# Optimization experiments

Measured on AMD Instinct MI355X. Metric: run time of the kernel, lower is better.

The kernel has to match this reference:

```python
import jax, jax.numpy as jnp
import numpy as np

N = 128   # system size (number of sequential RNN steps)
B = 8192  # batch of samples
H = 128   # hidden units per layer (units=[128,128])
D = 2     # input_dim (spin up/down one-hot)


def setup_inputs() -> dict:
    key = jax.random.key(0)
    ks = jax.random.split(key, 11)
    s = 1.0 / np.sqrt(H)  # torch nn.RNNCell/Linear default U(-1/sqrt(H), 1/sqrt(H))
    bits = jax.random.randint(ks[0], (N, B), 0, D)
    samples = jax.nn.one_hot(bits, D, dtype=jnp.float32)  # (N, B, D) one-hot spins
    u = lambda k, shp: jax.random.uniform(k, shp, jnp.float32, -s, s)
    return {
        "samples": samples,
        "W_ih0": u(ks[1], (H, D)), "b_ih0": u(ks[2], (H,)),
        "W_hh0": u(ks[3], (H, H)), "b_hh0": u(ks[4], (H,)),
        "W_ih1": u(ks[5], (H, H)), "b_ih1": u(ks[6], (H,)),
        "W_hh1": u(ks[7], (H, H)), "b_hh1": u(ks[8], (H,)),
        "W_dense": u(ks[9], (D, H)), "b_dense": u(ks[10], (D,)),
    }


def reference(samples, W_ih0, b_ih0, W_hh0, b_hh0,
              W_ih1, b_ih1, W_hh1, b_hh1, W_dense, b_dense):
    # Faithful jax port of RNN_wavefunction.log_prob:
    # p_t = <softmax(dense(h1_t)), s_t>; returns sum_t log p_t with shape (1, B).
    # For one-hot s_t, log(sum(prob*s_t)) == sum(s_t * log_softmax(logits)) (stable form).
    Bsz = samples.shape[1]
    # input at step t is the sampled spin from step t-1; zeros at t=0
    inputs = jnp.concatenate(
        [jnp.zeros((1, Bsz, D), samples.dtype), samples[:-1]], axis=0)
    h0 = jnp.zeros((Bsz, H), samples.dtype)
    h1 = jnp.zeros((Bsz, H), samples.dtype)

    def step(carry, xs):
        h0, h1 = carry
        x_t, s_t = xs  # x_t: (B, D) prev spin one-hot, s_t: (B, D) current spin
        # nn.RNNCell: h' = tanh(x W_ih^T + b_ih + h W_hh^T + b_hh)
        h0 = jnp.tanh(x_t @ W_ih0.T + b_ih0 + h0 @ W_hh0.T + b_hh0)
        h1 = jnp.tanh(h0 @ W_ih1.T + b_ih1 + h1 @ W_hh1.T + b_hh1)
        logits = h1 @ W_dense.T + b_dense           # (B, 2)
        logp = jax.nn.log_softmax(logits, axis=-1)
        lp_t = jnp.sum(logp * s_t, axis=-1)          # (B,) = log p(s_t)
        return (h0, h1), lp_t

    _, lps = jax.lax.scan(step, (h0, h1), (inputs, samples))  # lps: (N, B)
    return jnp.sum(lps, axis=0, keepdims=True)  # (1, B), matches torch keepdim=True
```

## Files before the change

### kernel.cpp

```cpp
#include <hip/hip_runtime.h>
#include <hip/hip_bf16.h>


#define NSTEP 128
#define BTOT  8192
#define HID   128
#define MB    16
#define NBLK  (BTOT / MB)
#define NTHR  256

typedef __attribute__((ext_vector_type(8))) short bf16x8;
typedef __attribute__((ext_vector_type(4))) float f32x4;
typedef __attribute__((ext_vector_type(2))) float f32x2;
typedef __attribute__((ext_vector_type(2))) unsigned uint32x2;

__device__ __forceinline__ short f2bf(float v) {
    unsigned u = __builtin_bit_cast(unsigned, v);
    u += 0x7FFFu + ((u >> 16) & 1u);
    return (short)(u >> 16);
}
__device__ __forceinline__ unsigned pk2bf(float a, float b) {
    unsigned ua = __builtin_bit_cast(unsigned, a);
    unsigned ub = __builtin_bit_cast(unsigned, b);
    ua += 0x7FFFu + ((ua >> 16) & 1u);
    ub += 0x7FFFu + ((ub >> 16) & 1u);
    return (ua >> 16) | (ub & 0xFFFF0000u);
}
__device__ __forceinline__ f32x2 tanh2(f32x2 x) {
    f32x2 z = x * 2.885390081777927f;
    f32x2 e;
    e.x = __builtin_exp2f(z.x);
    e.y = __builtin_exp2f(z.y);
    f32x2 d = e + 1.0f;
    f32x2 r;
    r.x = __builtin_amdgcn_rcpf(d.x);
    r.y = __builtin_amdgcn_rcpf(d.y);
    return r * -2.0f + 1.0f;
}

__global__ __launch_bounds__(NTHR, 2) void rnn_wf_kernel(
    const float* __restrict__ samples,
    const float* __restrict__ Wih0,
    const float* __restrict__ bih0,
    const float* __restrict__ Whh0,
    const float* __restrict__ bhh0,
    const float* __restrict__ Wih1,
    const float* __restrict__ bih1,
    const float* __restrict__ Whh1,
    const float* __restrict__ bhh1,
    const float* __restrict__ Wd,
    const float* __restrict__ bd,
    float* __restrict__ out)
{
    __shared__ short sH0[2][MB * HID];
    __shared__ short sH1[2][MB * HID];
    __shared__ unsigned sMask[NSTEP];

    const int tid  = threadIdx.x;
    const int b0   = blockIdx.x * MB;
    const int w    = tid >> 6;
    const int lane = tid & 63;
    const int q    = lane >> 4;
    const int c    = lane & 15;
    const int nb   = w * 32;

    if (tid < NSTEP) {
        unsigned msk = 0;
        #pragma unroll
        for (int m = 0; m < MB; ++m) {
            float e1 = samples[((size_t)tid * BTOT + b0 + m) * 2 + 1];
            if (e1 > 0.5f) msk |= (1u << m);
        }
        sMask[tid] = msk;
    }

    bf16x8 fhh0[2][4], fih1[2][4], fhh1[2][4];
    #pragma unroll
    for (int nt = 0; nt < 2; ++nt) {
        const int nn = nb + nt * 16 + c;
        #pragma unroll
        for (int kb = 0; kb < 4; ++kb) {
            const int off = nn * HID + kb * 32 + q * 8;
            bf16x8 v0, v1, v2;
            #pragma unroll
            for (int j = 0; j < 8; ++j) {
                v0[j] = f2bf(Whh0[off + j]);
                v1[j] = f2bf(Wih1[off + j]);
                v2[j] = f2bf(Whh1[off + j]);
            }
            fhh0[nt][kb] = v0; fih1[nt][kb] = v1; fhh1[nt][kb] = v2;
        }
    }
    bf16x8 fwd[4];
    #pragma unroll
    for (int kb = 0; kb < 4; ++kb) {
        bf16x8 v;
        #pragma unroll
        for (int j = 0; j < 8; ++j)
            v[j] = (c < 2) ? f2bf(Wd[c * HID + kb * 32 + q * 8 + j]) : (short)0;
        fwd[kb] = v;
    }
    f32x4 pA0, pA1, pB0, pB1, b0v0, b0v1, b1v0, b1v1;
    #pragma unroll
    for (int r = 0; r < 4; ++r) {
        const int n0 = nb + q * 4 + r;
        const int n1 = n0 + 16;
        const float bb0 = bih0[n0] + bhh0[n0];
        const float bb1 = bih0[n1] + bhh0[n1];
        b0v0[r] = bb0;                    b0v1[r] = bb1;
        pA0[r] = bb0 + Wih0[n0 * 2 + 0];  pA1[r] = bb1 + Wih0[n1 * 2 + 0];
        pB0[r] = bb0 + Wih0[n0 * 2 + 1];  pB1[r] = bb1 + Wih0[n1 * 2 + 1];
        b1v0[r] = bih1[n0] + bhh1[n0];    b1v1[r] = bih1[n1] + bhh1[n1];
    }
    const f32x4 bdv = {bd[0], bd[1], 0.f, 0.f};

    int ra[4];
    #pragma unroll
    for (int kb = 0; kb < 4; ++kb)
        ra[kb] = c * HID + (((kb * 4 + q) ^ c) << 3);
    int wa0 = c * HID + (((4 * w + (q >> 1)) ^ c) << 3) + ((q & 1) << 2);
    int wa1 = c * HID + (((4 * w + 2 + (q >> 1)) ^ c) << 3) + ((q & 1) << 2);

    float lp = 0.0f;
    bool bmPrev = false;

    auto storeH = [&](short* buf, const f32x4& a0, const f32x4& a1) {
        f32x2 t00 = tanh2((f32x2){a0[0], a0[1]});
        f32x2 t01 = tanh2((f32x2){a0[2], a0[3]});
        f32x2 t10 = tanh2((f32x2){a1[0], a1[1]});
        f32x2 t11 = tanh2((f32x2){a1[2], a1[3]});
        uint32x2 v0 = {pk2bf(t00.x, t00.y), pk2bf(t01.x, t01.y)};
        uint32x2 v1 = {pk2bf(t10.x, t10.y), pk2bf(t11.x, t11.y)};
        *reinterpret_cast<uint32x2*>(&buf[wa0]) = v0;
        *reinterpret_cast<uint32x2*>(&buf[wa1]) = v1;
    };
    auto lpAdd = [&](const f32x4& aL, bool bit) {
        const float l0 = aL[0], l1 = aL[1];
        const float lc = bit ? l1 : l0;
        const float lo = bit ? l0 : l1;
        const float ed = __builtin_exp2f((lo - lc) * 1.4426950408889634f);
        lp -= 0.6931471805599453f * __builtin_log2f(1.0f + ed);
    };

    __syncthreads();
    storeH(sH0[1], b0v0, b0v1);
    __syncthreads();

    {
        const bool bmIn = (sMask[0] >> c) & 1u;
        bf16x8 f0[4];
        #pragma unroll
        for (int kb = 0; kb < 4; ++kb)
            f0[kb] = *reinterpret_cast<const bf16x8*>(&sH0[1][ra[kb]]);
        f32x4 a00 = bmIn ? pB0 : pA0;
        f32x4 a01 = bmIn ? pB1 : pA1;
        f32x4 a10 = b1v0, a11 = b1v1;
        #pragma unroll
        for (int kb = 0; kb < 4; ++kb) {
            a00 = __builtin_amdgcn_mfma_f32_16x16x32_bf16(fhh0[0][kb], f0[kb], a00, 0, 0, 0);
            a01 = __builtin_amdgcn_mfma_f32_16x16x32_bf16(fhh0[1][kb], f0[kb], a01, 0, 0, 0);
            a10 = __builtin_amdgcn_mfma_f32_16x16x32_bf16(fih1[0][kb], f0[kb], a10, 0, 0, 0);
            a11 = __builtin_amdgcn_mfma_f32_16x16x32_bf16(fih1[1][kb], f0[kb], a11, 0, 0, 0);
        }
        storeH(sH0[0], a00, a01);
        storeH(sH1[0], a10, a11);
        bmPrev = bmIn;
        __syncthreads();
    }

    auto stepMain = [&](int i, const short* r0, const short* r1,
                        short* w0b, short* w1b) {
        const bool bmIn = (sMask[i - 1] >> c) & 1u;
        bf16x8 f0[4], f1[4];
        #pragma unroll
        for (int kb = 0; kb < 4; ++kb) {
            f0[kb] = *reinterpret_cast<const bf16x8*>(&r0[ra[kb]]);
            f1[kb] = *reinterpret_cast<const bf16x8*>(&r1[ra[kb]]);
        }
        f32x4 a00 = bmIn ? pB0 : pA0;
        f32x4 a01 = bmIn ? pB1 : pA1;
        f32x4 a10 = b1v0, a11 = b1v1;
        f32x4 aL  = bdv;
        #pragma unroll
        for (int kb = 0; kb < 4; ++kb) {
            a00 = __builtin_amdgcn_mfma_f32_16x16x32_bf16(fhh0[0][kb], f0[kb], a00, 0, 0, 0);
            a01 = __builtin_amdgcn_mfma_f32_16x16x32_bf16(fhh0[1][kb], f0[kb], a01, 0, 0, 0);
            a10 = __builtin_amdgcn_mfma_f32_16x16x32_bf16(fhh1[0][kb], f1[kb], a10, 0, 0, 0);
            a11 = __builtin_amdgcn_mfma_f32_16x16x32_bf16(fhh1[1][kb], f1[kb], a11, 0, 0, 0);
            aL  = __builtin_amdgcn_mfma_f32_16x16x32_bf16(fwd[kb],     f1[kb], aL,  0, 0, 0);
        }
        #pragma unroll
        for (int kb = 0; kb < 4; ++kb) {
            a10 = __builtin_amdgcn_mfma_f32_16x16x32_bf16(fih1[0][kb], f0[kb], a10, 0, 0, 0);
            a11 = __builtin_amdgcn_mfma_f32_16x16x32_bf16(fih1[1][kb], f0[kb], a11, 0, 0, 0);
        }
        lpAdd(aL, bmPrev);
        bmPrev = bmIn;
        storeH(w0b, a00, a01);
        storeH(w1b, a10, a11);
        __syncthreads();
    };

    for (int i = 2; i < NSTEP; i += 2) {
        stepMain(i,     sH0[0], sH1[0], sH0[1], sH1[1]);
        stepMain(i + 1, sH0[1], sH1[1], sH0[0], sH1[0]);
    }

    {
        bf16x8 f0[4], f1[4];
        #pragma unroll
        for (int kb = 0; kb < 4; ++kb) {
            f0[kb] = *reinterpret_cast<const bf16x8*>(&sH0[0][ra[kb]]);
            f1[kb] = *reinterpret_cast<const bf16x8*>(&sH1[0][ra[kb]]);
        }
        f32x4 a10 = b1v0, a11 = b1v1;
        f32x4 aL  = bdv;
        #pragma unroll
        for (int kb = 0; kb < 4; ++kb) {
            a10 = __builtin_amdgcn_mfma_f32_16x16x32_bf16(fhh1[0][kb], f1[kb], a10, 0, 0, 0);
            a11 = __builtin_amdgcn_mfma_f32_16x16x32_bf16(fhh1[1][kb], f1[kb], a11, 0, 0, 0);
            aL  = __builtin_amdgcn_mfma_f32_16x16x32_bf16(fwd[kb],     f1[kb], aL,  0, 0, 0);
        }
        #pragma unroll
        for (int kb = 0; kb < 4; ++kb) {
            a10 = __builtin_amdgcn_mfma_f32_16x16x32_bf16(fih1[0][kb], f0[kb], a10, 0, 0, 0);
            a11 = __builtin_amdgcn_mfma_f32_16x16x32_bf16(fih1[1][kb], f0[kb], a11, 0, 0, 0);
        }
        lpAdd(aL, bmPrev);
        storeH(sH1[1], a10, a11);
        __syncthreads();
    }
    {
        f32x4 aL = bdv;
        #pragma unroll
        for (int kb = 0; kb < 4; ++kb) {
            bf16x8 f1 = *reinterpret_cast<const bf16x8*>(&sH1[1][ra[kb]]);
            aL = __builtin_amdgcn_mfma_f32_16x16x32_bf16(fwd[kb], f1, aL, 0, 0, 0);
        }
        lpAdd(aL, (sMask[NSTEP - 1] >> c) & 1u);
    }

    if (tid < 16)
        out[b0 + tid] = lp;
}

extern "C" void kernel_launch(void* const* d_in, const int* in_sizes, int n_in,
                              void* d_out, int out_size, void* d_ws, size_t ws_size,
                              hipStream_t stream) {
    rnn_wf_kernel<<<NBLK, NTHR, 0, stream>>>(
        (const float*)d_in[0],
        (const float*)d_in[1],
        (const float*)d_in[2],
        (const float*)d_in[3],
        (const float*)d_in[4],
        (const float*)d_in[5],
        (const float*)d_in[6],
        (const float*)d_in[7],
        (const float*)d_in[8],
        (const float*)d_in[9],
        (const float*)d_in[10],
        (float*)d_out);
}
```

Measured before the change: 263.2 us.

## Restrict dense logits to one wave and defer log-softmax to a parallel epilogue

Only wave 0 now computes the dense-layer MFMA each step, and it stores the logit difference to a shared buffer instead of doing exp/log on the serial critical path. A final epilogue spreads the 128 softplus evaluations per sample across all threads and reduces them with shuffles. The change also fuses the bias init into the first MFMA, swaps manual bf16 packing for the HIP packed conversion intrinsic, and shares one reciprocal across two tanh values. It adds about 8.7KB of LDS, which may affect occupancy, and introduces wave divergence inside each step.

```diff
diff --git a/kernel.cpp b/kernel.cpp
--- a/kernel.cpp
+++ b/kernel.cpp
@@ -19,23 +19,19 @@
     u += 0x7FFFu + ((u >> 16) & 1u);
     return (short)(u >> 16);
 }
-__device__ __forceinline__ unsigned pk2bf(float a, float b) {
-    unsigned ua = __builtin_bit_cast(unsigned, a);
-    unsigned ub = __builtin_bit_cast(unsigned, b);
-    ua += 0x7FFFu + ((ua >> 16) & 1u);
-    ub += 0x7FFFu + ((ub >> 16) & 1u);
-    return (ua >> 16) | (ub & 0xFFFF0000u);
+__device__ __forceinline__ unsigned cvt2bf(float a, float b) {
+    __hip_bfloat162 h2 = __float22bfloat162_rn(make_float2(a, b));
+    unsigned u; __builtin_memcpy(&u, &h2, sizeof(u));
+    return u;
 }
 __device__ __forceinline__ f32x2 tanh2(f32x2 x) {
     f32x2 z = x * 2.885390081777927f;
-    f32x2 e;
-    e.x = __builtin_exp2f(z.x);
-    e.y = __builtin_exp2f(z.y);
-    f32x2 d = e + 1.0f;
-    f32x2 r;
-    r.x = __builtin_amdgcn_rcpf(d.x);
-    r.y = __builtin_amdgcn_rcpf(d.y);
-    return r * -2.0f + 1.0f;
+    float e0 = __builtin_exp2f(z.x);
+    float e1 = __builtin_exp2f(z.y);
+    f32x2 d = {e0 + 1.0f, e1 + 1.0f};
+    float r = __builtin_amdgcn_rcpf(d.x * d.y);
+    f32x2 inv = {r * d.y, r * d.x};
+    return inv * -2.0f + 1.0f;
 }
 
 __global__ __launch_bounds__(NTHR, 2) void rnn_wf_kernel(
@@ -55,6 +51,7 @@
     __shared__ short sH0[2][MB * HID];
     __shared__ short sH1[2][MB * HID];
     __shared__ unsigned sMask[NSTEP];
+    __shared__ float sLd[NSTEP * 17];
 
     const int tid  = threadIdx.x;
     const int b0   = blockIdx.x * MB;
@@ -118,10 +115,9 @@
     #pragma unroll
     for (int kb = 0; kb < 4; ++kb)
         ra[kb] = c * HID + (((kb * 4 + q) ^ c) << 3);
-    int wa0 = c * HID + (((4 * w + (q >> 1)) ^ c) << 3) + ((q & 1) << 2);
-    int wa1 = c * HID + (((4 * w + 2 + (q >> 1)) ^ c) << 3) + ((q & 1) << 2);
-
-    float lp = 0.0f;
+    const int wa0 = c * HID + (((4 * w + (q >> 1)) ^ c) << 3) + ((q & 1) << 2);
+    const int wa1 = c * HID + (((4 * w + 2 + (q >> 1)) ^ c) << 3) + ((q & 1) << 2);
+
     bool bmPrev = false;
 
     auto storeH = [&](short* buf, const f32x4& a0, const f32x4& a1) {
@@ -129,18 +125,11 @@
         f32x2 t01 = tanh2((f32x2){a0[2], a0[3]});
         f32x2 t10 = tanh2((f32x2){a1[0], a1[1]});
         f32x2 t11 = tanh2((f32x2){a1[2], a1[3]});
-        uint32x2 v0 = {pk2bf(t00.x, t00.y), pk2bf(t01.x, t01.y)};
-        uint32x2 v1 = {pk2bf(t10.x, t10.y), pk2bf(t11.x, t11.y)};
+        uint32x2 v0 = {cvt2bf(t00.x, t00.y), cvt2bf(t01.x, t01.y)};
+        uint32x2 v1 = {cvt2bf(t10.x, t10.y), cvt2bf(t11.x, t11.y)};
         *reinterpret_cast<uint32x2*>(&buf[wa0]) = v0;
         *reinterpret_cast<uint32x2*>(&buf[wa1]) = v1;
     };
-    auto lpAdd = [&](const f32x4& aL, bool bit) {
-        const float l0 = aL[0], l1 = aL[1];
-        const float lc = bit ? l1 : l0;
-        const float lo = bit ? l0 : l1;
-        const float ed = __builtin_exp2f((lo - lc) * 1.4426950408889634f);
-        lp -= 0.6931471805599453f * __builtin_log2f(1.0f + ed);
-    };
 
     __syncthreads();
     storeH(sH0[1], b0v0, b0v1);
@@ -152,11 +141,12 @@
         #pragma unroll
         for (int kb = 0; kb < 4; ++kb)
             f0[kb] = *reinterpret_cast<const bf16x8*>(&sH0[1][ra[kb]]);
-        f32x4 a00 = bmIn ? pB0 : pA0;
-        f32x4 a01 = bmIn ? pB1 : pA1;
-        f32x4 a10 = b1v0, a11 = b1v1;
-        #pragma unroll
-        for (int kb = 0; kb < 4; ++kb) {
+        f32x4 a00 = __builtin_amdgcn_mfma_f32_16x16x32_bf16(fhh0[0][0], f0[0], bmIn ? pB0 : pA0, 0, 0, 0);
+        f32x4 a01 = __builtin_amdgcn_mfma_f32_16x16x32_bf16(fhh0[1][0], f0[0], bmIn ? pB1 : pA1, 0, 0, 0);
+        f32x4 a10 = __builtin_amdgcn_mfma_f32_16x16x32_bf16(fih1[0][0], f0[0], b1v0, 0, 0, 0);
+        f32x4 a11 = __builtin_amdgcn_mfma_f32_16x16x32_bf16(fih1[1][0], f0[0], b1v1, 0, 0, 0);
+        #pragma unroll
+        for (int kb = 1; kb < 4; ++kb) {
             a00 = __builtin_amdgcn_mfma_f32_16x16x32_bf16(fhh0[0][kb], f0[kb], a00, 0, 0, 0);
             a01 = __builtin_amdgcn_mfma_f32_16x16x32_bf16(fhh0[1][kb], f0[kb], a01, 0, 0, 0);
             a10 = __builtin_amdgcn_mfma_f32_16x16x32_bf16(fih1[0][kb], f0[kb], a10, 0, 0, 0);
@@ -177,24 +167,30 @@
             f0[kb] = *reinterpret_cast<const bf16x8*>(&r0[ra[kb]]);
             f1[kb] = *reinterpret_cast<const bf16x8*>(&r1[ra[kb]]);
         }
-        f32x4 a00 = bmIn ? pB0 : pA0;
-        f32x4 a01 = bmIn ? pB1 : pA1;
-        f32x4 a10 = b1v0, a11 = b1v1;
-        f32x4 aL  = bdv;
-        #pragma unroll
-        for (int kb = 0; kb < 4; ++kb) {
+        f32x4 a00 = __builtin_amdgcn_mfma_f32_16x16x32_bf16(fhh0[0][0], f0[0], bmIn ? pB0 : pA0, 0, 0, 0);
+        f32x4 a01 = __builtin_amdgcn_mfma_f32_16x16x32_bf16(fhh0[1][0], f0[0], bmIn ? pB1 : pA1, 0, 0, 0);
+        f32x4 a10 = __builtin_amdgcn_mfma_f32_16x16x32_bf16(fhh1[0][0], f1[0], b1v0, 0, 0, 0);
+        f32x4 a11 = __builtin_amdgcn_mfma_f32_16x16x32_bf16(fhh1[1][0], f1[0], b1v1, 0, 0, 0);
+        #pragma unroll
+        for (int kb = 1; kb < 4; ++kb) {
             a00 = __builtin_amdgcn_mfma_f32_16x16x32_bf16(fhh0[0][kb], f0[kb], a00, 0, 0, 0);
             a01 = __builtin_amdgcn_mfma_f32_16x16x32_bf16(fhh0[1][kb], f0[kb], a01, 0, 0, 0);
             a10 = __builtin_amdgcn_mfma_f32_16x16x32_bf16(fhh1[0][kb], f1[kb], a10, 0, 0, 0);
             a11 = __builtin_amdgcn_mfma_f32_16x16x32_bf16(fhh1[1][kb], f1[kb], a11, 0, 0, 0);
-            aL  = __builtin_amdgcn_mfma_f32_16x16x32_bf16(fwd[kb],     f1[kb], aL,  0, 0, 0);
         }
         #pragma unroll
         for (int kb = 0; kb < 4; ++kb) {
             a10 = __builtin_amdgcn_mfma_f32_16x16x32_bf16(fih1[0][kb], f0[kb], a10, 0, 0, 0);
             a11 = __builtin_amdgcn_mfma_f32_16x16x32_bf16(fih1[1][kb], f0[kb], a11, 0, 0, 0);
         }
-        lpAdd(aL, bmPrev);
+        if (w == 0) {
+            f32x4 aL = __builtin_amdgcn_mfma_f32_16x16x32_bf16(fwd[0], f1[0], bdv, 0, 0, 0);
+            #pragma unroll
+            for (int kb = 1; kb < 4; ++kb)
+                aL = __builtin_amdgcn_mfma_f32_16x16x32_bf16(fwd[kb], f1[kb], aL, 0, 0, 0);
+            if (q == 0)
+                sLd[(i - 2) * 17 + c] = bmPrev ? (aL[0] - aL[1]) : (aL[1] - aL[0]);
+        }
         bmPrev = bmIn;
         storeH(w0b, a00, a01);
         storeH(w1b, a10, a11);
@@ -213,35 +209,63 @@
             f0[kb] = *reinterpret_cast<const bf16x8*>(&sH0[0][ra[kb]]);
             f1[kb] = *reinterpret_cast<const bf16x8*>(&sH1[0][ra[kb]]);
         }
-        f32x4 a10 = b1v0, a11 = b1v1;
-        f32x4 aL  = bdv;
-        #pragma unroll
-        for (int kb = 0; kb < 4; ++kb) {
+        f32x4 a10 = __builtin_amdgcn_mfma_f32_16x16x32_bf16(fhh1[0][0], f1[0], b1v0, 0, 0, 0);
+        f32x4 a11 = __builtin_amdgcn_mfma_f32_16x16x32_bf16(fhh1[1][0], f1[0], b1v1, 0, 0, 0);
+        #pragma unroll
+        for (int kb = 1; kb < 4; ++kb) {
             a10 = __builtin_amdgcn_mfma_f32_16x16x32_bf16(fhh1[0][kb], f1[kb], a10, 0, 0, 0);
             a11 = __builtin_amdgcn_mfma_f32_16x16x32_bf16(fhh1[1][kb], f1[kb], a11, 0, 0, 0);
-            aL  = __builtin_amdgcn_mfma_f32_16x16x32_bf16(fwd[kb],     f1[kb], aL,  0, 0, 0);
         }
         #pragma unroll
         for (int kb = 0; kb < 4; ++kb) {
             a10 = __builtin_amdgcn_mfma_f32_16x16x32_bf16(fih1[0][kb], f0[kb], a10, 0, 0, 0);
             a11 = __builtin_amdgcn_mfma_f32_16x16x32_bf16(fih1[1][kb], f0[kb], a11, 0, 0, 0);
         }
-        lpAdd(aL, bmPrev);
+        if (w == 0) {
+            f32x4 aL = __builtin_amdgcn_mfma_f32_16x16x32_bf16(fwd[0], f1[0], bdv, 0, 0, 0);
+            #pragma unroll
+            for (int kb = 1; kb < 4; ++kb)
+                aL = __builtin_amdgcn_mfma_f32_16x16x32_bf16(fwd[kb], f1[kb], aL, 0, 0, 0);
+            if (q == 0)
+                sLd[126 * 17 + c] = bmPrev ? (aL[0] - aL[1]) : (aL[1] - aL[0]);
+        }
         storeH(sH1[1], a10, a11);
         __syncthreads();
     }
-    {
-        f32x4 aL = bdv;
-        #pragma unroll
-        for (int kb = 0; kb < 4; ++kb) {
+    if (w == 0) {
+        f32x4 aL;
+        {
+            bf16x8 f1 = *reinterpret_cast<const bf16x8*>(&sH1[1][ra[0]]);
+            aL = __builtin_amdgcn_mfma_f32_16x16x32_bf16(fwd[0], f1, bdv, 0, 0, 0);
+        }
+        #pragma unroll
+        for (int kb = 1; kb < 4; ++kb) {
             bf16x8 f1 = *reinterpret_cast<const bf16x8*>(&sH1[1][ra[kb]]);
             aL = __builtin_amdgcn_mfma_f32_16x16x32_bf16(fwd[kb], f1, aL, 0, 0, 0);
         }
-        lpAdd(aL, (sMask[NSTEP - 1] >> c) & 1u);
-    }
-
-    if (tid < 16)
-        out[b0 + tid] = lp;
+        if (q == 0) {
+            const bool bit = (sMask[NSTEP - 1] >> c) & 1u;
+            sLd[127 * 17 + c] = bit ? (aL[0] - aL[1]) : (aL[1] - aL[0]);
+        }
+    }
+    __syncthreads();
+
+    {
+        const int s = tid >> 4;
+        const int k = tid & 15;
+        float acc = 0.0f;
+        #pragma unroll
+        for (int j = 0; j < 8; ++j) {
+            const float x = sLd[(j * 16 + k) * 17 + s];
+            const float ed = __builtin_exp2f(x * 1.4426950408889634f);
+            acc -= 0.6931471805599453f * __builtin_log2f(1.0f + ed);
+        }
+        #pragma unroll
+        for (int off = 1; off < 16; off <<= 1)
+            acc += __shfl_xor(acc, off, 64);
+        if (k == 0)
+            out[b0 + s] = acc;
+    }
 }
 
 extern "C" void kernel_launch(void* const* d_in, const int* in_sizes, int n_in,
```

Result: no change. 258.6 us (-1.8%).
